# Kernel optimization log

Hardware: AMD Instinct MI355X
Metric: run time of the kernel (lower is better)

The kernel has to match this reference:

```python
import math
import jax, jax.numpy as jnp
import numpy as np

DIM = 192
HEADS = 4
OUT_DIM = 192

def _conv(x, w, groups=1, pad=0):
    return jax.lax.conv_general_dilated(
        x, w, window_strides=(1, 1), padding=[(pad, pad), (pad, pad)],
        feature_group_count=groups, dimension_numbers=('NCHW', 'OIHW', 'NCHW'))

def setup_inputs() -> dict:
    key = jax.random.key(0)
    ks = jax.random.split(key, 8)
    b, c, h, w = 8, DIM, 128, 128
    x = jax.random.normal(ks[0], (b, c, h, w), dtype=jnp.float32)
    y = jax.random.normal(ks[1], (b, c, h, w), dtype=jnp.float32)
    s = 0.02
    kv_w = jax.random.normal(ks[2], (2 * DIM, DIM, 1, 1), dtype=jnp.float32) * s
    kv_dw_w = jax.random.normal(ks[3], (2 * DIM, 1, 3, 3), dtype=jnp.float32) * s  # depthwise, groups=2*dim
    q_w = jax.random.normal(ks[4], (DIM, DIM, 1, 1), dtype=jnp.float32) * s
    q_dw_w = jax.random.normal(ks[5], (DIM, DIM, 3, 3), dtype=jnp.float32) * s  # dense 3x3 (groups=1 in source)
    proj_w = jax.random.normal(ks[6], (OUT_DIM, DIM, 1, 1), dtype=jnp.float32) * s
    temperature = jnp.ones((HEADS, 1, 1), dtype=jnp.float32)
    return {"x": x, "y": y, "kv_w": kv_w, "kv_dw_w": kv_dw_w, "q_w": q_w,
            "q_dw_w": q_dw_w, "proj_w": proj_w, "temperature": temperature}

def _l2norm(t, eps=1e-12):
    # matches torch F.normalize(dim=-1)
    n = jnp.sqrt(jnp.sum(t * t, axis=-1, keepdims=True))
    return t / jnp.maximum(n, eps)

def reference(x, y, kv_w, kv_dw_w, q_w, q_dw_w, proj_w, temperature):
    b, c, h, w = x.shape
    hw = h * w
    ch = c // HEADS  # channels per head
    kv = _conv(_conv(x, kv_w), kv_dw_w, groups=2 * c, pad=1)  # [b, 2c, h, w]
    k, v = jnp.split(kv, 2, axis=1)
    q = _conv(_conv(y, q_w), q_dw_w, pad=1)  # [b, c, h, w]
    # b (head ch) h w -> b head ch (h w)
    q = q.reshape(b, HEADS, ch, hw)
    k = k.reshape(b, HEADS, ch, hw)
    v = v.reshape(b, HEADS, ch, hw)
    q = _l2norm(q)
    k = _l2norm(k)
    attn = jnp.einsum('bhcn,bhdn->bhcd', q, k)  # channel-wise attention [b,H,ch,ch]
    temp = temperature * math.log(attn.shape[-1])  # [H,1,1]
    attn = jax.nn.softmax(attn * temp[None], axis=-1)
    out = jnp.einsum('bhcd,bhdn->bhcn', attn, v)  # [b,H,ch,hw]
    out = out.reshape(b, c, h, w)
    return _conv(out, proj_w)
```

## Files before the change

kernel.cpp:

```cpp
#include <hip/hip_runtime.h>


#define HW 16384

using f32x4  = __attribute__((ext_vector_type(4))) float;
using bf16x8 = __attribute__((ext_vector_type(8))) __bf16;
using u16x8  = __attribute__((ext_vector_type(8))) unsigned short;
typedef unsigned short u16;

__device__ __forceinline__ u16 f2bf(float f) {
  unsigned u = __builtin_bit_cast(unsigned, f);
  u = (u + 0x7fffu + ((u >> 16) & 1u)) >> 16;
  return (u16)u;
}
__device__ __forceinline__ float bf2f(u16 s) {
  unsigned u = ((unsigned)s) << 16;
  return __builtin_bit_cast(float, u);
}

__device__ __forceinline__ void g2l16(const void* g, void* l) {
  __builtin_amdgcn_global_load_lds(
      (const __attribute__((address_space(1))) unsigned int*)g,
      (__attribute__((address_space(3))) unsigned int*)l, 16, 0, 0);
}

__global__ __launch_bounds__(256) void pack_w1(
    const float* __restrict__ kv_w, u16* __restrict__ W1) {
  int i = blockIdx.x * 256 + threadIdx.x;
  W1[i] = f2bf(kv_w[i]);
}

__global__ __launch_bounds__(192) void make_w4(
    const float* __restrict__ q_w, const float* __restrict__ q_dw_w,
    u16* __restrict__ W4) {
  const int o = blockIdx.x / 9, seg = blockIdx.x % 9;
  const int c = threadIdx.x;
  float s = 0.f;
  for (int ic = 0; ic < 192; ++ic)
    s += q_dw_w[(o * 192 + ic) * 9 + seg] * q_w[ic * 192 + c];
  W4[o * 1728 + seg * 192 + c] = f2bf(s);
}

template <typename TIn>
__global__ __launch_bounds__(256) void transpose_kernel(
    const TIn* __restrict__ src, u16* __restrict__ dst, int srcCstride) {
  __shared__ u16 tile[32][34];
  const int bz = blockIdx.z;
  const int n0 = blockIdx.x * 32;
  const int c0 = blockIdx.y * 32;
  const TIn* s = src + (long)bz * srcCstride * HW;
  u16* d = dst + (long)bz * HW * 192;
  const int tx = threadIdx.x & 31;
  const int ty = threadIdx.x >> 5;
#pragma unroll
  for (int i = 0; i < 32; i += 8) {
    if constexpr (sizeof(TIn) == 4)
      tile[ty + i][tx] = f2bf(((const float*)s)[(long)(c0 + ty + i) * HW + n0 + tx]);
    else
      tile[ty + i][tx] = ((const u16*)s)[(long)(c0 + ty + i) * HW + n0 + tx];
  }
  __syncthreads();
#pragma unroll
  for (int i = 0; i < 32; i += 8)
    d[(long)(n0 + ty + i) * 192 + c0 + tx] = tile[tx][ty + i];
}

template <int NSEG, bool OUT_BF16, bool FUSE_RQ>
__global__ __launch_bounds__(512, 2) void gemm_kernel(
    const u16* __restrict__ A, const u16* __restrict__ Bt,
    void* __restrict__ Cout, const u16* __restrict__ zp,
    int M, long aBatchStride, float* __restrict__ rqs) {
  __shared__ __align__(16) u16 shA[2][12288];
  __shared__ __align__(16) u16 shB[2][16384];
  const int Ktot = NSEG * 192;
  const int NT = NSEG * 3;
  const int tid = threadIdx.x;
  const int w = tid >> 6;
  const int lane = tid & 63;
  const int rl = lane & 15;
  const int q4 = lane >> 4;
  const int wm = w >> 2, wn = w & 3;
  const int b = blockIdx.z;
  const int n0 = blockIdx.x * 256;
  const int m0 = blockIdx.y * 192;

  const u16* Ab = A + (long)b * aBatchStride + (long)m0 * Ktot;
  const u16* Btb = Bt + (long)b * HW * 192;
  const char* zpp = (const char*)zp + q4 * 16;

  const char* aptr0 = (const char*)(Ab + (long)(w * 16 + rl) * Ktot) + q4 * 16;
  const char* aptr1 = (const char*)(Ab + (long)((8 + (w >> 1)) * 16 + rl) * Ktot)
                      + q4 * 16 + (w & 1) * 64;

  const char* p0b[2];
  int xx[2], yy[2];
#pragma unroll
  for (int jj = 0; jj < 2; ++jj) {
    int n = n0 + (2 * w + jj) * 16 + rl;
    p0b[jj] = (const char*)(Btb + (long)n * 192) + q4 * 16;
    xx[jj] = n & 127;
    yy[jj] = n >> 7;
  }

  f32x4 acc[6][4];
#pragma unroll
  for (int i = 0; i < 6; ++i)
#pragma unroll
    for (int j = 0; j < 4; ++j) acc[i][j] = f32x4{0.f, 0.f, 0.f, 0.f};

  const int lane_off = lane * 8;

  auto stage = [&](int tt, int sbuf) {
    u16* dA = &shA[sbuf][0];
    u16* dB = &shB[sbuf][0];
    const long ao = (long)tt * 128;
    g2l16(aptr0 + ao,      dA + (w * 2 + 0) * 512);
    g2l16(aptr0 + ao + 64, dA + (w * 2 + 1) * 512);
    g2l16(aptr1 + ao,      dA + ((8 + (w >> 1)) * 2 + (w & 1)) * 512);
    if constexpr (NSEG == 1) {
      const long kb = (long)tt * 128;
#pragma unroll
      for (int jj = 0; jj < 2; ++jj) {
        g2l16(p0b[jj] + kb,      dB + ((2 * w + jj) * 2 + 0) * 512);
        g2l16(p0b[jj] + kb + 64, dB + ((2 * w + jj) * 2 + 1) * 512);
      }
    } else {
      const int seg = tt / 3;
      const long kb = (long)(tt - seg * 3) * 128;
      const int dy = seg / 3 - 1, dx = seg % 3 - 1;
      const long roff = (long)(dy * 128 + dx) * 384;
#pragma unroll
      for (int jj = 0; jj < 2; ++jj) {
        bool ok = ((unsigned)(xx[jj] + dx) < 128u) && ((unsigned)(yy[jj] + dy) < 128u);
        const char* bp = ok ? p0b[jj] + roff : zpp;
        g2l16(bp + kb,      dB + ((2 * w + jj) * 2 + 0) * 512);
        g2l16(bp + kb + 64, dB + ((2 * w + jj) * 2 + 1) * 512);
      }
    }
  };

  auto compute = [&](int cbuf) {
    const u16* sA = &shA[cbuf][0];
    const u16* sB = &shB[cbuf][0];
    bf16x8 af[6][2];
#pragma unroll
    for (int i = 0; i < 6; ++i)
#pragma unroll
      for (int h = 0; h < 2; ++h)
        af[i][h] = *(const bf16x8*)&sA[((wm * 6 + i) * 2 + h) * 512 + lane_off];
    bf16x8 bfr[4][2];
#pragma unroll
    for (int j = 0; j < 4; ++j)
#pragma unroll
      for (int h = 0; h < 2; ++h)
        bfr[j][h] = *(const bf16x8*)&sB[((wn * 4 + j) * 2 + h) * 512 + lane_off];
#pragma unroll
    for (int i = 0; i < 6; ++i)
#pragma unroll
      for (int j = 0; j < 4; ++j) {
        acc[i][j] = __builtin_amdgcn_mfma_f32_16x16x32_bf16(af[i][0], bfr[j][0], acc[i][j], 0, 0, 0);
        acc[i][j] = __builtin_amdgcn_mfma_f32_16x16x32_bf16(af[i][1], bfr[j][1], acc[i][j], 0, 0, 0);
      }
  };

  stage(0, 0);
  stage(1, 1);
  for (int t = 0; t < NT; ++t) {
    const int cur = t & 1;
    if (t < NT - 1)
      asm volatile("s_waitcnt vmcnt(7)" ::: "memory");
    else
      asm volatile("s_waitcnt vmcnt(0)" ::: "memory");
    __builtin_amdgcn_s_barrier();
    compute(cur);
    asm volatile("s_waitcnt lgkmcnt(0)" ::: "memory");
    __builtin_amdgcn_sched_barrier(0);
    __builtin_amdgcn_s_barrier();
    if (t + 2 < NT) stage(t + 2, cur);
  }

  const int mb = m0 + wm * 96;
  const int nb = n0 + wn * 64;
  if constexpr (OUT_BF16) {
    u16* Cb = (u16*)Cout + (long)b * M * HW;
#pragma unroll
    for (int i = 0; i < 6; ++i)
#pragma unroll
      for (int j = 0; j < 4; ++j)
#pragma unroll
        for (int r = 0; r < 4; ++r)
          Cb[(long)(mb + i * 16 + q4 * 4 + r) * HW + nb + j * 16 + rl] = f2bf(acc[i][j][r]);
  } else {
    float* Cb = (float*)Cout + (long)b * M * HW;
#pragma unroll
    for (int i = 0; i < 6; ++i)
#pragma unroll
      for (int j = 0; j < 4; ++j)
#pragma unroll
        for (int r = 0; r < 4; ++r)
          Cb[(long)(mb + i * 16 + q4 * 4 + r) * HW + nb + j * 16 + rl] = acc[i][j][r];
  }
  if constexpr (FUSE_RQ) {
#pragma unroll
    for (int i = 0; i < 6; ++i)
#pragma unroll
      for (int r = 0; r < 4; ++r) {
        float s = 0.f;
#pragma unroll
        for (int j = 0; j < 4; ++j) s += acc[i][j][r] * acc[i][j][r];
        s += __shfl_xor(s, 1, 64);
        s += __shfl_xor(s, 2, 64);
        s += __shfl_xor(s, 4, 64);
        s += __shfl_xor(s, 8, 64);
        if (rl == 0)
          atomicAdd(&rqs[b * 192 + mb + i * 16 + q4 * 4 + r], s);
      }
  }
}

template <bool FUSE_NORM>
__global__ __launch_bounds__(256) void dwconv_kernel(
    const u16* __restrict__ kv, const float* __restrict__ dww,
    u16* __restrict__ dst, int cbase, int dstCstride, float* __restrict__ rks) {
  __shared__ __align__(16) u16 sp[HW];
  const int c = blockIdx.x;
  const int b = blockIdx.y;
  const int c2 = cbase + c;
  const u16* src = kv + ((long)b * 384 + c2) * HW;
  u16* out = dst + ((long)b * dstCstride + c) * HW;
  const int tid = threadIdx.x;
#pragma unroll
  for (int it = 0; it < 8; ++it)
    ((u16x8*)sp)[it * 256 + tid] = ((const u16x8*)src)[it * 256 + tid];
  __syncthreads();
  float w9[9];
#pragma unroll
  for (int t = 0; t < 9; ++t) w9[t] = dww[c2 * 9 + t];
  float ssum = 0.f;
  for (int o = 0; o < 8; ++o) {
    const int base = o * 2048 + tid * 8;
    const int yy = base >> 7;
    const int x0 = base & 127;
    float vv[3][10];
#pragma unroll
    for (int r = 0; r < 3; ++r) {
      int yr = yy + r - 1;
      if (yr >= 0 && yr < 128) {
        const u16* rp = sp + yr * 128 + x0;
        u16x8 mid = *(const u16x8*)rp;
#pragma unroll
        for (int i2 = 0; i2 < 8; ++i2) vv[r][1 + i2] = bf2f(mid[i2]);
        vv[r][0] = (x0 > 0)   ? bf2f(rp[-1]) : 0.f;
        vv[r][9] = (x0 < 120) ? bf2f(rp[8])  : 0.f;
      } else {
#pragma unroll
        for (int i2 = 0; i2 < 10; ++i2) vv[r][i2] = 0.f;
      }
    }
    u16x8 ov;
#pragma unroll
    for (int i2 = 0; i2 < 8; ++i2) {
      float s = 0.f;
#pragma unroll
      for (int r = 0; r < 3; ++r)
#pragma unroll
        for (int d = 0; d < 3; ++d) s += w9[r * 3 + d] * vv[r][i2 + d];
      if constexpr (FUSE_NORM) ssum += s * s;
      ov[i2] = f2bf(s);
    }
    *(u16x8*)(out + base) = ov;
  }
  if constexpr (FUSE_NORM) {
#pragma unroll
    for (int off = 32; off; off >>= 1) ssum += __shfl_down(ssum, off, 64);
    if ((tid & 63) == 0) atomicAdd(&rks[b * 192 + c], ssum);
  }
}

__global__ __launch_bounds__(256) void gram_kernel(
    const u16* __restrict__ qq, const u16* __restrict__ kk, float* __restrict__ gram) {
  __shared__ float red[4 * 2304];
  const int bh = blockIdx.x;
  const int kc = blockIdx.y;
  const int b = bh >> 2, h = bh & 3;
  const u16* qb = qq + ((long)b * 192 + h * 48) * HW;
  const u16* kb = kk + ((long)b * 192 + h * 48) * HW;
  const int tid = threadIdx.x, w = tid >> 6, lane = tid & 63;
  const int rl = lane & 15, q4 = lane >> 4;
  f32x4 acc[3][3];
#pragma unroll
  for (int i = 0; i < 3; ++i)
#pragma unroll
    for (int j = 0; j < 3; ++j) acc[i][j] = f32x4{0.f, 0.f, 0.f, 0.f};
  for (int tt = 0; tt < 16; ++tt) {
    const int k0 = ((kc * 16 + tt) * 4 + w) * 32 + q4 * 8;
    bf16x8 af[3], bfr[3];
#pragma unroll
    for (int i = 0; i < 3; ++i) af[i] = *(const bf16x8*)(qb + (long)(i * 16 + rl) * HW + k0);
#pragma unroll
    for (int j = 0; j < 3; ++j) bfr[j] = *(const bf16x8*)(kb + (long)(j * 16 + rl) * HW + k0);
#pragma unroll
    for (int i = 0; i < 3; ++i)
#pragma unroll
      for (int j = 0; j < 3; ++j)
        acc[i][j] = __builtin_amdgcn_mfma_f32_16x16x32_bf16(af[i], bfr[j], acc[i][j], 0, 0, 0);
  }
#pragma unroll
  for (int i = 0; i < 3; ++i)
#pragma unroll
    for (int j = 0; j < 3; ++j)
#pragma unroll
      for (int r = 0; r < 4; ++r)
        red[w * 2304 + (i * 16 + q4 * 4 + r) * 48 + j * 16 + rl] = acc[i][j][r];
  __syncthreads();
  for (int e = tid; e < 2304; e += 256)
    atomicAdd(&gram[(long)bh * 2304 + e], red[e] + red[2304 + e] + red[4608 + e] + red[6912 + e]);
}

__global__ __launch_bounds__(64) void softmax_kernel(
    const float* __restrict__ gram, const float* __restrict__ rqs,
    const float* __restrict__ rks, const float* __restrict__ temperature,
    float* __restrict__ attn) {
  const int R = blockIdx.x;
  const int lane = threadIdx.x;
  const int b = R / 192;
  const int h = (R % 192) / 48;
  const float ts = temperature[h] * 3.8712010109078907f;
  const float rq = rsqrtf(fmaxf(rqs[R], 1e-24f));
  float val = -3.0e38f;
  if (lane < 48) {
    const float rk = rsqrtf(fmaxf(rks[b * 192 + h * 48 + lane], 1e-24f));
    val = gram[(long)R * 48 + lane] * rq * rk * ts;
  }
  float mx = val;
#pragma unroll
  for (int off = 32; off; off >>= 1) mx = fmaxf(mx, __shfl_xor(mx, off, 64));
  float ex = (lane < 48) ? expf(val - mx) : 0.f;
  float sm = ex;
#pragma unroll
  for (int off = 32; off; off >>= 1) sm += __shfl_xor(sm, off, 64);
  if (lane < 48) attn[(long)R * 48 + lane] = ex / sm;
}

__global__ __launch_bounds__(192) void pa_kernel(
    const float* __restrict__ proj_w, const float* __restrict__ attn,
    u16* __restrict__ PA) {
  const int b = blockIdx.x;
  const int o = blockIdx.y;
  const int dg = threadIdx.x;
  const int hg = dg / 48, dl = dg % 48;
  const float* arow = attn + ((long)(b * 4 + hg) * 48) * 48 + dl;
  const float* prow = proj_w + o * 192 + hg * 48;
  float s = 0.f;
#pragma unroll
  for (int cl = 0; cl < 48; ++cl) s += prow[cl] * arow[(long)cl * 48];
  PA[((long)b * 192 + o) * 192 + dg] = f2bf(s);
}

extern "C" void kernel_launch(void* const* d_in, const int* in_sizes, int n_in,
                              void* d_out, int out_size, void* d_ws, size_t ws_size,
                              hipStream_t stream) {
  (void)in_sizes; (void)n_in; (void)out_size; (void)ws_size;
  const float* x        = (const float*)d_in[0];
  const float* y        = (const float*)d_in[1];
  const float* kv_w     = (const float*)d_in[2];
  const float* kv_dw_w  = (const float*)d_in[3];
  const float* q_w      = (const float*)d_in[4];
  const float* q_dw_w   = (const float*)d_in[5];
  const float* proj_w   = (const float*)d_in[6];
  const float* temperature = (const float*)d_in[7];

  char* ws = (char*)d_ws;
  u16* KV = (u16*)(ws + 0L);
  u16* R0 = (u16*)(ws + 100663296L);
  u16* R1 = (u16*)(ws + 150994944L);
  u16* R2 = (u16*)(ws + 201326592L);
  char* tail = ws + 251658240L;
  u16*   zp   = (u16*)(tail + 0);
  float* rqs  = (float*)(tail + 512);
  float* rks  = (float*)(tail + 6656);
  float* gram = (float*)(tail + 12800);
  float* attn = (float*)(tail + 307712);
  u16*   W1   = (u16*)(tail + 602624);
  u16*   W4   = (u16*)(tail + 750080);
  u16*   PA   = (u16*)(tail + 1413632);

  hipMemsetAsync(tail, 0, 307712, stream);
  pack_w1<<<288, 256, 0, stream>>>(kv_w, W1);
  make_w4<<<1728, 192, 0, stream>>>(q_w, q_dw_w, W4);

  transpose_kernel<float><<<dim3(512, 6, 8), 256, 0, stream>>>(y, R2, 192);
  gemm_kernel<9, true, true><<<dim3(64, 1, 8), 512, 0, stream>>>(W4, R2, R1, zp, 192, 0, rqs);

  transpose_kernel<float><<<dim3(512, 6, 8), 256, 0, stream>>>(x, R2, 192);
  gemm_kernel<1, true, false><<<dim3(64, 2, 8), 512, 0, stream>>>(W1, R2, KV, zp, 384, 0, nullptr);
  dwconv_kernel<true><<<dim3(192, 8), 256, 0, stream>>>(KV, kv_dw_w, R0, 0, 192, rks);
  dwconv_kernel<false><<<dim3(192, 8), 256, 0, stream>>>(KV, kv_dw_w, KV, 192, 384, nullptr);
  transpose_kernel<u16><<<dim3(512, 6, 8), 256, 0, stream>>>(KV, R2, 384);

  gram_kernel<<<dim3(32, 8), 256, 0, stream>>>(R1, R0, gram);
  softmax_kernel<<<1536, 64, 0, stream>>>(gram, rqs, rks, temperature, attn);
  pa_kernel<<<dim3(8, 192), 192, 0, stream>>>(proj_w, attn, PA);
  gemm_kernel<1, false, false><<<dim3(64, 1, 8), 512, 0, stream>>>(PA, R2, d_out, zp, 192, 36864, nullptr);
}
```

Measured before the change: 643.1 us.

## Restructure GEMM mainloop into 4-stage ring buffer with split-phase MFMA and prefetch

```diff
diff --git a/kernel.cpp b/kernel.cpp
--- a/kernel.cpp
+++ b/kernel.cpp
@@ -70,10 +70,9 @@
     const u16* __restrict__ A, const u16* __restrict__ Bt,
     void* __restrict__ Cout, const u16* __restrict__ zp,
     int M, long aBatchStride, float* __restrict__ rqs) {
-  __shared__ __align__(16) u16 shA[2][12288];
-  __shared__ __align__(16) u16 shB[2][16384];
+  __shared__ __align__(16) u16 sh[57344];
+  constexpr int NT = NSEG * 6;
   const int Ktot = NSEG * 192;
-  const int NT = NSEG * 3;
   const int tid = threadIdx.x;
   const int w = tid >> 6;
   const int lane = tid & 63;
@@ -87,19 +86,19 @@
   const u16* Ab = A + (long)b * aBatchStride + (long)m0 * Ktot;
   const u16* Btb = Bt + (long)b * HW * 192;
   const char* zpp = (const char*)zp + q4 * 16;
-
-  const char* aptr0 = (const char*)(Ab + (long)(w * 16 + rl) * Ktot) + q4 * 16;
-  const char* aptr1 = (const char*)(Ab + (long)((8 + (w >> 1)) * 16 + rl) * Ktot)
-                      + q4 * 16 + (w & 1) * 64;
-
-  const char* p0b[2];
-  int xx[2], yy[2];
+  const bool hasA2 = (w < 4);
+
+  const char* asrcA  = (const char*)(Ab + (long)(w * 16 + rl) * Ktot) + q4 * 16;
+  const char* asrcA2 = (const char*)(Ab + (long)(128 + w * 16 + rl) * Ktot) + q4 * 16;
+
+  const char* bsrc0[2];
+  int bx[2], by[2];
 #pragma unroll
   for (int jj = 0; jj < 2; ++jj) {
     int n = n0 + (2 * w + jj) * 16 + rl;
-    p0b[jj] = (const char*)(Btb + (long)n * 192) + q4 * 16;
-    xx[jj] = n & 127;
-    yy[jj] = n >> 7;
+    bsrc0[jj] = (const char*)(Btb + (long)n * 192) + q4 * 16;
+    bx[jj] = n & 127;
+    by[jj] = n >> 7;
   }
 
   f32x4 acc[6][4];
@@ -108,75 +107,88 @@
 #pragma unroll
     for (int j = 0; j < 4; ++j) acc[i][j] = f32x4{0.f, 0.f, 0.f, 0.f};
 
-  const int lane_off = lane * 8;
-
-  auto stage = [&](int tt, int sbuf) {
-    u16* dA = &shA[sbuf][0];
-    u16* dB = &shB[sbuf][0];
-    const long ao = (long)tt * 128;
-    g2l16(aptr0 + ao,      dA + (w * 2 + 0) * 512);
-    g2l16(aptr0 + ao + 64, dA + (w * 2 + 1) * 512);
-    g2l16(aptr1 + ao,      dA + ((8 + (w >> 1)) * 2 + (w & 1)) * 512);
+  const int lo = lane * 8;
+
+  auto stageA = [&](int kt) {
+    u16* base = sh + (kt & 3) * 14336;
+    const long ak = (long)kt * 64;
+    g2l16(asrcA + ak, base + w * 512);
+    if (hasA2) g2l16(asrcA2 + ak, base + (8 + w) * 512);
+  };
+  auto stageB = [&](int kt) {
+    u16* base = sh + (kt & 3) * 14336 + 6144;
     if constexpr (NSEG == 1) {
-      const long kb = (long)tt * 128;
-#pragma unroll
-      for (int jj = 0; jj < 2; ++jj) {
-        g2l16(p0b[jj] + kb,      dB + ((2 * w + jj) * 2 + 0) * 512);
-        g2l16(p0b[jj] + kb + 64, dB + ((2 * w + jj) * 2 + 1) * 512);
-      }
+      const long bk = (long)kt * 64;
+      g2l16(bsrc0[0] + bk, base + (2 * w) * 512);
+      g2l16(bsrc0[1] + bk, base + (2 * w + 1) * 512);
     } else {
-      const int seg = tt / 3;
-      const long kb = (long)(tt - seg * 3) * 128;
+      const int seg = kt / 6;
+      const long bk = (long)(kt - seg * 6) * 64;
       const int dy = seg / 3 - 1, dx = seg % 3 - 1;
       const long roff = (long)(dy * 128 + dx) * 384;
 #pragma unroll
       for (int jj = 0; jj < 2; ++jj) {
-        bool ok = ((unsigned)(xx[jj] + dx) < 128u) && ((unsigned)(yy[jj] + dy) < 128u);
-        const char* bp = ok ? p0b[jj] + roff : zpp;
-        g2l16(bp + kb,      dB + ((2 * w + jj) * 2 + 0) * 512);
-        g2l16(bp + kb + 64, dB + ((2 * w + jj) * 2 + 1) * 512);
+        bool ok = ((unsigned)(bx[jj] + dx) < 128u) && ((unsigned)(by[jj] + dy) < 128u);
+        const char* bp = ok ? bsrc0[jj] + roff : zpp;
+        g2l16(bp + bk, base + (2 * w + jj) * 512);
       }
     }
   };
 
-  auto compute = [&](int cbuf) {
-    const u16* sA = &shA[cbuf][0];
-    const u16* sB = &shB[cbuf][0];
-    bf16x8 af[6][2];
-#pragma unroll
-    for (int i = 0; i < 6; ++i)
-#pragma unroll
-      for (int h = 0; h < 2; ++h)
-        af[i][h] = *(const bf16x8*)&sA[((wm * 6 + i) * 2 + h) * 512 + lane_off];
-    bf16x8 bfr[4][2];
+  stageA(0); stageB(0);
+  stageA(1); stageB(1);
+  stageA(2); stageB(2);
+  if (hasA2) asm volatile("s_waitcnt vmcnt(8)" ::: "memory");
+  else       asm volatile("s_waitcnt vmcnt(6)" ::: "memory");
+  __builtin_amdgcn_s_barrier();
+
+  for (int kt = 0; kt < NT; ++kt) {
+    const u16* base = sh + (kt & 3) * 14336;
+    const u16* baseB = base + 6144;
+    bf16x8 af0[3], bfv[4];
+#pragma unroll
+    for (int i = 0; i < 3; ++i)
+      af0[i] = *(const bf16x8*)&base[(wm * 6 + i) * 512 + lo];
 #pragma unroll
     for (int j = 0; j < 4; ++j)
-#pragma unroll
-      for (int h = 0; h < 2; ++h)
-        bfr[j][h] = *(const bf16x8*)&sB[((wn * 4 + j) * 2 + h) * 512 + lane_off];
-#pragma unroll
-    for (int i = 0; i < 6; ++i)
-#pragma unroll
-      for (int j = 0; j < 4; ++j) {
-        acc[i][j] = __builtin_amdgcn_mfma_f32_16x16x32_bf16(af[i][0], bfr[j][0], acc[i][j], 0, 0, 0);
-        acc[i][j] = __builtin_amdgcn_mfma_f32_16x16x32_bf16(af[i][1], bfr[j][1], acc[i][j], 0, 0, 0);
-      }
-  };
-
-  stage(0, 0);
-  stage(1, 1);
-  for (int t = 0; t < NT; ++t) {
-    const int cur = t & 1;
-    if (t < NT - 1)
-      asm volatile("s_waitcnt vmcnt(7)" ::: "memory");
-    else
-      asm volatile("s_waitcnt vmcnt(0)" ::: "memory");
+      bfv[j] = *(const bf16x8*)&baseB[(wn * 4 + j) * 512 + lo];
+    if (kt + 3 < NT) stageA(kt + 3);
     __builtin_amdgcn_s_barrier();
-    compute(cur);
     asm volatile("s_waitcnt lgkmcnt(0)" ::: "memory");
     __builtin_amdgcn_sched_barrier(0);
+    __builtin_amdgcn_s_setprio(1);
+#pragma unroll
+    for (int i = 0; i < 3; ++i)
+#pragma unroll
+      for (int j = 0; j < 4; ++j)
+        acc[i][j] = __builtin_amdgcn_mfma_f32_16x16x32_bf16(af0[i], bfv[j], acc[i][j], 0, 0, 0);
+    __builtin_amdgcn_s_setprio(0);
     __builtin_amdgcn_s_barrier();
-    if (t + 2 < NT) stage(t + 2, cur);
+    bf16x8 af1[3];
+#pragma unroll
+    for (int i = 0; i < 3; ++i)
+      af1[i] = *(const bf16x8*)&base[(wm * 6 + 3 + i) * 512 + lo];
+    if (kt + 3 < NT) stageB(kt + 3);
+    if (kt <= NT - 4) {
+      if (hasA2) asm volatile("s_waitcnt vmcnt(8)" ::: "memory");
+      else       asm volatile("s_waitcnt vmcnt(6)" ::: "memory");
+    } else if (kt == NT - 3) {
+      if (hasA2) asm volatile("s_waitcnt vmcnt(4)" ::: "memory");
+      else       asm volatile("s_waitcnt vmcnt(3)" ::: "memory");
+    } else if (kt == NT - 2) {
+      asm volatile("s_waitcnt vmcnt(0)" ::: "memory");
+    }
+    __builtin_amdgcn_s_barrier();
+    asm volatile("s_waitcnt lgkmcnt(0)" ::: "memory");
+    __builtin_amdgcn_sched_barrier(0);
+    __builtin_amdgcn_s_setprio(1);
+#pragma unroll
+    for (int i = 0; i < 3; ++i)
+#pragma unroll
+      for (int j = 0; j < 4; ++j)
+        acc[3 + i][j] = __builtin_amdgcn_mfma_f32_16x16x32_bf16(af1[i], bfv[j], acc[3 + i][j], 0, 0, 0);
+    __builtin_amdgcn_s_setprio(0);
+    __builtin_amdgcn_s_barrier();
   }
 
   const int mb = m0 + wm * 96;
```

After: 591.1 us. 8.1% less time.
